# Performance work log

Measured on AMD Instinct MI355X. Metric: run time of the kernel, lower is better.

The kernel has to match this reference:

```python
import jax, jax.numpy as jnp
import numpy as np

B, S, E, H = 2, 2048, 1024, 16
D = E // H  # head_dim = 64

def setup_inputs() -> dict:
    key = jax.random.key(0)
    ks = jax.random.split(key, 11)
    s = 1.0 / np.sqrt(E)
    inp = {
        'query': jax.random.normal(ks[0], (B, S, E), jnp.float32),
        'key':   jax.random.normal(ks[1], (B, S, E), jnp.float32),
        'value': jax.random.normal(ks[2], (B, S, E), jnp.float32),
        'Wq': jax.random.uniform(ks[3], (E, E), jnp.float32, -s, s),
        'bq': jax.random.uniform(ks[4], (E,), jnp.float32, -s, s),
        'Wk': jax.random.uniform(ks[5], (E, E), jnp.float32, -s, s),
        'bk': jax.random.uniform(ks[6], (E,), jnp.float32, -s, s),
        'Wv': jax.random.uniform(ks[7], (E, E), jnp.float32, -s, s),
        'bv': jax.random.uniform(ks[8], (E,), jnp.float32, -s, s),
        'Wo': jax.random.uniform(ks[9], (E, E), jnp.float32, -s, s),
        'bo': jax.random.uniform(ks[10], (E,), jnp.float32, -s, s),
    }
    return inp

def reference(query, key, value, Wq, bq, Wk, bk, Wv, bv, Wo, bo):
    # project and split heads: [B,S,E] -> [B,H,S,D]
    def proj(x, W, b):
        y = jnp.einsum('bse,fe->bsf', x, W) + b  # torch Linear: x @ W.T + b
        return y.reshape(B, S, H, D).transpose(0, 2, 1, 3)
    q = proj(query, Wq, bq)
    k = proj(key, Wk, bk)
    v = proj(value, Wv, bv)
    scores = jnp.einsum('bhqd,bhkd->bhqk', q, k) / jnp.sqrt(jnp.float32(D))
    attn = jax.nn.softmax(scores, axis=-1)
    out = jnp.einsum('bhqk,bhkd->bhqd', attn, v)  # [B,H,S,D]
    out = out.transpose(0, 2, 1, 3).reshape(B, S, E)
    return jnp.einsum('bse,fe->bsf', out, Wo) + bo
```

## Files before the change

### kernel.cpp

```cpp
#include <hip/hip_runtime.h>

#define B_ 2
#define S_ 2048
#define E_ 1024
#define H_ 16
#define D_ 64
#define M_ (B_*S_)
#define K_ E_

typedef __attribute__((ext_vector_type(8))) short  short8;
typedef __attribute__((ext_vector_type(4))) float  f32x4;
typedef __attribute__((ext_vector_type(8))) unsigned short u16x8;
typedef __attribute__((ext_vector_type(4))) unsigned short u16x4;
typedef __attribute__((ext_vector_type(4))) unsigned int   u32x4;

#define QSCALE 0.18033688011112042f

#if __has_builtin(__builtin_amdgcn_exp2f)
#define EXP2F(x) __builtin_amdgcn_exp2f(x)
#else
#define EXP2F(x) exp2f(x)
#endif

__device__ __forceinline__ unsigned short f2bf(float f) {
    unsigned u = __float_as_uint(f);
    u += 0x7fffu + ((u >> 16) & 1u);
    return (unsigned short)(u >> 16);
}

__device__ __forceinline__ unsigned cvtpk(float a, float b) {
    unsigned r;
    asm("v_cvt_pk_bf16_f32 %0, %1, %2" : "=v"(r) : "v"(a), "v"(b));
    return r;
}

__device__ __forceinline__ void gl_lds16(const ushort* g, ushort* l) {
    __builtin_amdgcn_global_load_lds((const __attribute__((address_space(1))) void*)g,
                                     (__attribute__((address_space(3))) void*)l,
                                     16, 0, 0);
}

#define FL_SYNC(N) do {                                                   \
    asm volatile("s_waitcnt vmcnt(" #N ")" ::: "memory");                 \
    __builtin_amdgcn_s_barrier();                                         \
    asm volatile("" ::: "memory");                                        \
} while (0)

#define WAITL0_BAR() do {                                                 \
    asm volatile("s_waitcnt lgkmcnt(0)" ::: "memory");                    \
    __builtin_amdgcn_s_barrier();                                         \
    asm volatile("" ::: "memory");                                        \
} while (0)

__global__ __launch_bounds__(256)
void cvt_all(const float* __restrict__ q, const float* __restrict__ k,
             const float* __restrict__ v, const float* __restrict__ wq,
             const float* __restrict__ wk, const float* __restrict__ wv,
             const float* __restrict__ wo, ushort* __restrict__ dst)
{
    const int bid = blockIdx.x;
    const float* src;
    size_t dof;
    int local;
    if (bid < 6144) {
        const int t = bid >> 11;
        src = (t == 0) ? q : (t == 1) ? k : v;
        dof = (size_t)t * 4194304u;
        local = bid & 2047;
    } else {
        const int r = bid - 6144;
        const int t = r >> 9;
        src = (t == 0) ? wq : (t == 1) ? wk : (t == 2) ? wv : wo;
        dof = 12582912u + (size_t)t * 1048576u;
        local = r & 511;
    }
    const size_t idx = (size_t)local * 2048 + threadIdx.x * 8;
    const float4 a = *(const float4*)(src + idx);
    const float4 b = *(const float4*)(src + idx + 4);
    u16x8 o;
    o[0] = f2bf(a.x); o[1] = f2bf(a.y); o[2] = f2bf(a.z); o[3] = f2bf(a.w);
    o[4] = f2bf(b.x); o[5] = f2bf(b.y); o[6] = f2bf(b.z); o[7] = f2bf(b.w);
    *(u16x8*)(dst + dof + idx) = o;
}

template<int SWAP>
__device__ __forceinline__ void qkv_core(const ushort* __restrict__ X,
                                         const ushort* __restrict__ W,
                                         int m0, int n0,
                                         f32x4 acc[8][4], ushort* sh)
{
    const int tid  = threadIdx.x;
    const int lane = tid & 63;
    const int w    = tid >> 6;
    const int wm   = w & 1;
    const int wn   = w >> 1;
    const int l15  = lane & 15, quad = lane >> 4;

    const int srow = lane >> 3, schunk = lane & 7;
    const int scol = (schunk ^ srow) * 8;
    const ushort* pa[4]; const ushort* pb[4]; int loff[4];
    #pragma unroll
    for (int i = 0; i < 4; ++i) {
        const int row = (w * 4 + i) * 8 + srow;
        pa[i] = X + (size_t)(m0 + row) * K_ + scol;
        pb[i] = W + (size_t)(n0 + row) * K_ + scol;
        loff[i] = (w * 4 + i) * 512 + lane * 8;
    }

    const f32x4 zero = {0.f, 0.f, 0.f, 0.f};
    #pragma unroll
    for (int mt = 0; mt < 8; ++mt)
        #pragma unroll
        for (int nt = 0; nt < 4; ++nt) acc[mt][nt] = zero;

    #pragma unroll
    for (int i = 0; i < 4; ++i) {
        gl_lds16(pa[i],      sh + loff[i]);
        gl_lds16(pb[i],      sh + 16384 + loff[i]);
    }
    #pragma unroll
    for (int i = 0; i < 4; ++i) {
        gl_lds16(pa[i] + 64, sh + 32768 + loff[i]);
        gl_lds16(pb[i] + 64, sh + 32768 + 16384 + loff[i]);
    }

    const int arow = wm * 128 + l15;
    const int brow = wn * 64 + l15;

    for (int t = 0; t < 16; ++t) {
        ushort* curA = sh + (t & 1) * 32768;
        ushort* curB = curA + 16384;

        if (t < 15) { FL_SYNC(8); } else { FL_SYNC(0); }

        __builtin_amdgcn_s_setprio(1);
        #pragma unroll
        for (int kc = 0; kc < 2; ++kc) {
            short8 bf[4];
            #pragma unroll
            for (int nt = 0; nt < 4; ++nt) {
                const int r = brow + nt * 16;
                bf[nt] = *(const short8*)(curB + r * 64 + (((kc * 4 + quad) ^ (r & 7)) * 8));
            }
            #pragma unroll
            for (int mt = 0; mt < 8; ++mt) {
                const int r = arow + mt * 16;
                const short8 af = *(const short8*)(curA + r * 64 + (((kc * 4 + quad) ^ (r & 7)) * 8));
                #pragma unroll
                for (int nt = 0; nt < 4; ++nt) {
                    if (SWAP)
                        acc[mt][nt] = __builtin_amdgcn_mfma_f32_16x16x32_bf16(bf[nt], af, acc[mt][nt], 0, 0, 0);
                    else
                        acc[mt][nt] = __builtin_amdgcn_mfma_f32_16x16x32_bf16(af, bf[nt], acc[mt][nt], 0, 0, 0);
                }
            }
        }
        __builtin_amdgcn_s_setprio(0);

        if (t + 2 < 16) {
            WAITL0_BAR();
            const int k0 = (t + 2) * 64;
            #pragma unroll
            for (int i = 0; i < 4; ++i) {
                gl_lds16(pa[i] + k0, curA + loff[i]);
                gl_lds16(pb[i] + k0, curB + loff[i]);
            }
        }
    }
}

__global__ __launch_bounds__(512, 2)
void gemm_qkv(const ushort* __restrict__ Xq, const ushort* __restrict__ Xk,
              const ushort* __restrict__ Xv, const ushort* __restrict__ Wq,
              const ushort* __restrict__ Wk, const ushort* __restrict__ Wv,
              const float* __restrict__ bq, const float* __restrict__ bk,
              const float* __restrict__ bv, ushort* __restrict__ Qh,
              ushort* __restrict__ Kh, ushort* __restrict__ Vt)
{
    __shared__ ushort sh[65536];
    const int z = blockIdx.z;
    const ushort* X = (z == 0) ? Xq : (z == 1) ? Xk : Xv;
    const ushort* W = (z == 0) ? Wq : (z == 1) ? Wk : Wv;
    const float* bias = (z == 0) ? bq : (z == 1) ? bk : bv;
    ushort* dst = (z == 0) ? Qh : (z == 1) ? Kh : Vt;

    const int m0 = blockIdx.y * 256, n0 = blockIdx.x * 256;
    f32x4 acc[8][4];
    const int lane = threadIdx.x & 63, w = threadIdx.x >> 6;
    const int wm = w & 1, wn = w >> 1;
    const int l15 = lane & 15, quad = lane >> 4;

    if (z < 2) {
        qkv_core<1>(X, W, m0, n0, acc, sh);
        const float qsc = (z == 0) ? QSCALE : 1.0f;
        #pragma unroll
        for (int nt = 0; nt < 4; ++nt) {
            const int nb = n0 + wn * 64 + nt * 16 + quad * 4;
            const int h = nb >> 6, d0 = nb & 63;
            const float4 b4 = *(const float4*)(bias + nb);
            const float bb4[4] = {b4.x, b4.y, b4.z, b4.w};
            #pragma unroll
            for (int mt = 0; mt < 8; ++mt) {
                const int tok = m0 + wm * 128 + mt * 16 + l15;
                const int b = tok >> 11, s = tok & (S_ - 1);
                u16x4 pk;
                #pragma unroll
                for (int r = 0; r < 4; ++r)
                    pk[r] = f2bf((acc[mt][nt][r] + bb4[r]) * qsc);
                *(u16x4*)&dst[(((size_t)(b * H_ + h) * S_) + s) * D_ + d0] = pk;
            }
        }
    } else {
        qkv_core<0>(X, W, m0, n0, acc, sh);
        float bias4[4];
        #pragma unroll
        for (int nt = 0; nt < 4; ++nt)
            bias4[nt] = bias[n0 + wn * 64 + nt * 16 + l15];
        #pragma unroll
        for (int mt = 0; mt < 8; ++mt) {
            const int mrow0 = m0 + wm * 128 + mt * 16 + (quad * 4);
            const int b = mrow0 >> 11;
            const int s0 = mrow0 & (S_ - 1);
            #pragma unroll
            for (int nt = 0; nt < 4; ++nt) {
                const int n = n0 + wn * 64 + nt * 16 + l15;
                const int h = n >> 6, d = n & 63;
                u16x4 pk;
                #pragma unroll
                for (int r = 0; r < 4; ++r) pk[r] = f2bf(acc[mt][nt][r] + bias4[nt]);
                *(u16x4*)&Vt[(((size_t)(b * H_ + h) * D_) + d) * S_ + s0] = pk;
            }
        }
    }
}

__global__ __launch_bounds__(256)
void gemm_out(const ushort* __restrict__ X, const ushort* __restrict__ W,
              const float* __restrict__ bias, float* __restrict__ out)
{
    __shared__ ushort sh[24576];
    const int m0 = blockIdx.y * 128, n0 = blockIdx.x * 64;
    const int tid = threadIdx.x, lane = tid & 63, w = tid >> 6;
    const int wm = w & 1, wn = w >> 1;
    const int l15 = lane & 15, quad = lane >> 4;
    const int r0 = tid >> 2, c8 = (tid & 3) * 8;
    const int kb = quad * 8;

    const ushort* ga = X + (size_t)(m0 + r0) * K_ + c8;
    const ushort* gb = W + (size_t)(n0 + r0) * K_ + c8;

    const f32x4 zero = {0.f, 0.f, 0.f, 0.f};
    f32x4 acc[4][2];
    #pragma unroll
    for (int mt = 0; mt < 4; ++mt)
        #pragma unroll
        for (int nt = 0; nt < 2; ++nt) acc[mt][nt] = zero;

    #pragma unroll
    for (int t0 = 0; t0 < 2; ++t0) {
        ushort* sb = sh + t0 * 6144;
        gl_lds16(ga + t0 * 32,                 sb + tid * 8);
        gl_lds16(ga + t0 * 32 + (size_t)64 * K_, sb + 2048 + tid * 8);
        gl_lds16(gb + t0 * 32,                 sb + 4096 + tid * 8);
    }

    for (int t = 0; t < 32; ++t) {
        ushort* sb = sh + (t & 3) * 6144;

        if (t < 31) { FL_SYNC(3); } else { FL_SYNC(0); }

        short8 af[4], bf[2];
        #pragma unroll
        for (int mt = 0; mt < 4; ++mt)
            af[mt] = *(const short8*)(sb + (wm * 64 + mt * 16 + l15) * 32 + kb);
        #pragma unroll
        for (int nt = 0; nt < 2; ++nt)
            bf[nt] = *(const short8*)(sb + 4096 + (wn * 32 + nt * 16 + l15) * 32 + kb);

        if (t + 2 < 32) {
            ushort* nb = sh + ((t + 2) & 3) * 6144;
            const int k0 = (t + 2) * 32;
            gl_lds16(ga + k0,                 nb + tid * 8);
            gl_lds16(ga + k0 + (size_t)64 * K_, nb + 2048 + tid * 8);
            gl_lds16(gb + k0,                 nb + 4096 + tid * 8);
        }

        __builtin_amdgcn_s_setprio(1);
        #pragma unroll
        for (int mt = 0; mt < 4; ++mt)
            #pragma unroll
            for (int nt = 0; nt < 2; ++nt)
                acc[mt][nt] = __builtin_amdgcn_mfma_f32_16x16x32_bf16(af[mt], bf[nt], acc[mt][nt], 0, 0, 0);
        __builtin_amdgcn_s_setprio(0);
    }

    float bias2[2];
    #pragma unroll
    for (int nt = 0; nt < 2; ++nt)
        bias2[nt] = bias[n0 + wn * 32 + nt * 16 + l15];

    #pragma unroll
    for (int mt = 0; mt < 4; ++mt) {
        const int mrow0 = m0 + wm * 64 + mt * 16 + quad * 4;
        #pragma unroll
        for (int nt = 0; nt < 2; ++nt) {
            const int n = n0 + wn * 32 + nt * 16 + l15;
            #pragma unroll
            for (int r = 0; r < 4; ++r)
                out[(size_t)(mrow0 + r) * E_ + n] = acc[mt][nt][r] + bias2[nt];
        }
    }
}

#define NTILE (S_ / 64)
#define QBLK 128

__device__ __forceinline__ void flash_stage(const ushort* __restrict__ Kg,
                                            const ushort* __restrict__ Vg,
                                            size_t qk_off, size_t vt_off,
                                            ushort* sh, int j,
                                            int row0, int gcol0, int row1, int gcol1,
                                            int chunk0, int chunk1, int lane)
{
    ushort* sb = sh + 8192 + (j & 3) * 8192;
    const int j0n = j * 64;
    gl_lds16(Kg + qk_off + (size_t)(j0n + row0) * D_ + gcol0 * 8, sb + chunk0 * 512 + lane * 8);
    gl_lds16(Vg + vt_off + (size_t)row0 * S_ + j0n + gcol0 * 8, sb + 4096 + chunk0 * 512 + lane * 8);
    gl_lds16(Kg + qk_off + (size_t)(j0n + row1) * D_ + gcol1 * 8, sb + chunk1 * 512 + lane * 8);
    gl_lds16(Vg + vt_off + (size_t)row1 * S_ + j0n + gcol1 * 8, sb + 4096 + chunk1 * 512 + lane * 8);
}

__global__ __launch_bounds__(256, 2)
void flash_mfma(const ushort* __restrict__ Qg, const ushort* __restrict__ Kg,
                const ushort* __restrict__ Vg, ushort* __restrict__ AO)
{
    __shared__ ushort sh[40960];
    ushort* Qs = sh;

    const int tid = threadIdx.x, lane = tid & 63, w = tid >> 6;
    const int l15 = lane & 15, quad = lane >> 4;
    const int q0 = blockIdx.x * QBLK, h = blockIdx.y, b = blockIdx.z;
    const size_t qk_off = (size_t)(b * H_ + h) * S_ * D_;
    const size_t vt_off = (size_t)(b * H_ + h) * D_ * S_;

    const int chunk0 = w, chunk1 = w + 4;
    const int row0 = chunk0 * 8 + (lane >> 3);
    const int row1 = chunk1 * 8 + (lane >> 3);
    const int gcol0 = (lane & 7) ^ (row0 & 7);
    const int gcol1 = (lane & 7) ^ (row1 & 7);

    #pragma unroll
    for (int i = 0; i < 4; ++i) {
        const int qc = w + i * 4;
        const int qrow = qc * 8 + (lane >> 3);
        const int qg = (lane & 7) ^ (qrow & 7);
        gl_lds16(Qg + qk_off + (size_t)(q0 + qrow) * D_ + qg * 8,
                 Qs + qc * 512 + lane * 8);
    }
    flash_stage(Kg, Vg, qk_off, vt_off, sh, 0, row0, gcol0, row1, gcol1, chunk0, chunk1, lane);
    flash_stage(Kg, Vg, qk_off, vt_off, sh, 1, row0, gcol0, row1, gcol1, chunk0, chunk1, lane);

    FL_SYNC(8);

    f32x4 o[4][4];
    #pragma unroll
    for (int g = 0; g < 4; ++g)
        #pragma unroll
        for (int nt = 0; nt < 4; ++nt) o[g][nt] = {0.f, 0.f, 0.f, 0.f};
    float lsum[4] = {0.f, 0.f, 0.f, 0.f};

    const int qh  = (w >> 1) * 64;
    const int kvb = (w & 1) * 32;
    const int x7  = l15 & 7;
    const int rowA = (kvb + l15) * 64;
    const int rowB = (kvb + 16 + l15) * 64;
    const int gA = ((w & 1) * 4 + (quad >> 1)) ^ x7;
    const int gB = ((w & 1) * 4 + 2 + (quad >> 1)) ^ x7;
    const f32x4 zero = {0.f, 0.f, 0.f, 0.f};

    for (int j = 0; j < NTILE; ++j) {
        const ushort* Kb = sh + 8192 + (j & 3) * 8192;
        const ushort* Vb = Kb + 4096;
        if (j < NTILE - 1) { FL_SYNC(4); } else { FL_SYNC(0); }

        const short8 ka0 = *(const short8*)&Kb[rowA + ((quad ^ x7) * 8)];
        const short8 ka1 = *(const short8*)&Kb[rowA + (((4 + quad) ^ x7) * 8)];
        const short8 ka2 = *(const short8*)&Kb[rowB + ((quad ^ x7) * 8)];
        const short8 ka3 = *(const short8*)&Kb[rowB + (((4 + quad) ^ x7) * 8)];
        uint2 vvA[4], vvB[4];
        #pragma unroll
        for (int nt = 0; nt < 4; ++nt) {
            vvA[nt] = *(const uint2*)&Vb[(nt * 16 + l15) * 64 + gA * 8 + (quad & 1) * 4];
            vvB[nt] = *(const uint2*)&Vb[(nt * 16 + l15) * 64 + gB * 8 + (quad & 1) * 4];
        }

        if (j < NTILE - 2)
            flash_stage(Kg, Vg, qk_off, vt_off, sh, j + 2,
                        row0, gcol0, row1, gcol1, chunk0, chunk1, lane);

        __builtin_amdgcn_s_setprio(1);
        uint2 paLo[4], paHi[4];
        #pragma unroll
        for (int g = 0; g < 4; ++g) {
            const int qr = (qh + g * 16 + l15) * 64;
            const short8 qg0 = *(const short8*)&Qs[qr + ((quad ^ x7) * 8)];
            const short8 qg1 = *(const short8*)&Qs[qr + (((4 + quad) ^ x7) * 8)];
            f32x4 t = __builtin_amdgcn_mfma_f32_16x16x32_bf16(ka0, qg0, zero, 0, 0, 0);
            t = __builtin_amdgcn_mfma_f32_16x16x32_bf16(ka1, qg1, t, 0, 0, 0);
            f32x4 u = __builtin_amdgcn_mfma_f32_16x16x32_bf16(ka2, qg0, zero, 0, 0, 0);
            u = __builtin_amdgcn_mfma_f32_16x16x32_bf16(ka3, qg1, u, 0, 0, 0);
            {
                const float p0 = EXP2F(t[0]), p1 = EXP2F(t[1]);
                const float p2 = EXP2F(t[2]), p3 = EXP2F(t[3]);
                lsum[g] += (p0 + p1) + (p2 + p3);
                paLo[g].x = cvtpk(p0, p1);
                paLo[g].y = cvtpk(p2, p3);
            }
            {
                const float p0 = EXP2F(u[0]), p1 = EXP2F(u[1]);
                const float p2 = EXP2F(u[2]), p3 = EXP2F(u[3]);
                lsum[g] += (p0 + p1) + (p2 + p3);
                paHi[g].x = cvtpk(p0, p1);
                paHi[g].y = cvtpk(p2, p3);
            }
        }

        short8 pa8[4];
        #pragma unroll
        for (int g = 0; g < 4; ++g) {
            u32x4 pk;
            pk[0] = paLo[g].x; pk[1] = paLo[g].y;
            pk[2] = paHi[g].x; pk[3] = paHi[g].y;
            pa8[g] = __builtin_bit_cast(short8, pk);
        }
        #pragma unroll
        for (int nt = 0; nt < 4; ++nt) {
            u32x4 vk;
            vk[0] = vvA[nt].x; vk[1] = vvA[nt].y;
            vk[2] = vvB[nt].x; vk[3] = vvB[nt].y;
            const short8 vb8 = __builtin_bit_cast(short8, vk);
            #pragma unroll
            for (int g = 0; g < 4; ++g)
                o[g][nt] = __builtin_amdgcn_mfma_f32_16x16x32_bf16(pa8[g], vb8, o[g][nt], 0, 0, 0);
        }
        __builtin_amdgcn_s_setprio(0);
    }

    #pragma unroll
    for (int g = 0; g < 4; ++g) {
        lsum[g] += __shfl_xor(lsum[g], 16);
        lsum[g] += __shfl_xor(lsum[g], 32);
    }
    __syncthreads();
    float* fb = (float*)sh;
    if (w & 1) {
        #pragma unroll
        for (int g = 0; g < 4; ++g) {
            #pragma unroll
            for (int nt = 0; nt < 4; ++nt)
                #pragma unroll
                for (int r = 0; r < 4; ++r)
                    fb[(w >> 1) * 4096 + g * 1024 + (nt * 4 + r) * 64 + lane] = o[g][nt][r];
            if (quad == 0) fb[8192 + (w >> 1) * 64 + g * 16 + l15] = lsum[g];
        }
    }
    __syncthreads();
    if (!(w & 1)) {
        #pragma unroll
        for (int g = 0; g < 4; ++g) {
            #pragma unroll
            for (int nt = 0; nt < 4; ++nt)
                #pragma unroll
                for (int r = 0; r < 4; ++r)
                    o[g][nt][r] += fb[(w >> 1) * 4096 + g * 1024 + (nt * 4 + r) * 64 + lane];
            lsum[g] += fb[8192 + (w >> 1) * 64 + g * 16 + l15];
        }
        #pragma unroll
        for (int g = 0; g < 4; ++g) {
            const float inv = 1.0f / lsum[g];
            float invr[4];
            #pragma unroll
            for (int r = 0; r < 4; ++r)
                invr[r] = __shfl(inv, (lane & 0x30) | (quad * 4 + r));
            #pragma unroll
            for (int nt = 0; nt < 4; ++nt) {
                const int e = h * 64 + nt * 16 + l15;
                #pragma unroll
                for (int r = 0; r < 4; ++r) {
                    const int s = q0 + qh + g * 16 + quad * 4 + r;
                    AO[(size_t)(b * S_ + s) * E_ + e] = f2bf(o[g][nt][r] * invr[r]);
                }
            }
        }
    }
}

extern "C" void kernel_launch(void* const* d_in, const int* in_sizes, int n_in,
                              void* d_out, int out_size, void* d_ws, size_t ws_size,
                              hipStream_t stream) {
    const float* query = (const float*)d_in[0];
    const float* key   = (const float*)d_in[1];
    const float* value = (const float*)d_in[2];
    const float* Wq = (const float*)d_in[3];
    const float* bq = (const float*)d_in[4];
    const float* Wk = (const float*)d_in[5];
    const float* bk = (const float*)d_in[6];
    const float* Wv = (const float*)d_in[7];
    const float* bv = (const float*)d_in[8];
    const float* Wo = (const float*)d_in[9];
    const float* bo = (const float*)d_in[10];
    float* out = (float*)d_out;

    ushort* ws = (ushort*)d_ws;
    ushort* Xq  = ws;
    ushort* Xk  = ws + 4194304u;
    ushort* Xv  = ws + 8388608u;
    ushort* Wqb = ws + 12582912u;
    ushort* Wkb = ws + 13631488u;
    ushort* Wvb = ws + 14680064u;
    ushort* Wob = ws + 15728640u;
    ushort* Qh  = ws + 16777216u;
    ushort* Kh  = ws + 20971520u;
    ushort* Vt  = ws + 25165824u;
    ushort* AO  = ws + 29360128u;

    cvt_all<<<8192, 256, 0, stream>>>(query, key, value, Wq, Wk, Wv, Wo, ws);
    gemm_qkv<<<dim3(4, 16, 3), 512, 0, stream>>>(Xq, Xk, Xv, Wqb, Wkb, Wvb,
                                                 bq, bk, bv, Qh, Kh, Vt);
    flash_mfma<<<dim3(S_ / QBLK, H_, B_), 256, 0, stream>>>(Qh, Kh, Vt, AO);
    gemm_out<<<dim3(16, 32), 256, 0, stream>>>(AO, Wob, bo, out);
}
```

Baseline: 210.0 us.

## Switch QKV GEMM to 4-stage K=32 LDS ring with early prefetch

The QKV projection GEMM mainloop moves from a double-buffered K=64 tile to a four-slot ring of K=32 tiles. Each iteration now loads all A/B fragments into registers first, then issues the global-to-LDS prefetch for stage t+2, then runs the MFMAs. This removes the trailing wait-and-barrier before each prefetch and lets loads overlap compute more. In exchange there are twice as many iterations and more sync points, and the fragments held in registers raise register pressure.

```diff
diff --git a/kernel.cpp b/kernel.cpp
--- a/kernel.cpp
+++ b/kernel.cpp
@@ -83,6 +83,15 @@
     *(u16x8*)(dst + dof + idx) = o;
 }
 
+#define QKV_STAGE(t) do {                                                  \
+    ushort* sb_ = sh + ((t) & 3) * 16384;                                  \
+    const int k0_ = (t) * 32;                                              \
+    gl_lds16(pa0 + k0_, sb_ + ld0);                                        \
+    gl_lds16(pa1 + k0_, sb_ + 4096 + ld0);                                 \
+    gl_lds16(pb0 + k0_, sb_ + 8192 + ld0);                                 \
+    gl_lds16(pb1 + k0_, sb_ + 12288 + ld0);                                \
+} while (0)
+
 template<int SWAP>
 __device__ __forceinline__ void qkv_core(const ushort* __restrict__ X,
                                          const ushort* __restrict__ W,
@@ -96,16 +105,13 @@
     const int wn   = w >> 1;
     const int l15  = lane & 15, quad = lane >> 4;
 
-    const int srow = lane >> 3, schunk = lane & 7;
-    const int scol = (schunk ^ srow) * 8;
-    const ushort* pa[4]; const ushort* pb[4]; int loff[4];
-    #pragma unroll
-    for (int i = 0; i < 4; ++i) {
-        const int row = (w * 4 + i) * 8 + srow;
-        pa[i] = X + (size_t)(m0 + row) * K_ + scol;
-        pb[i] = W + (size_t)(n0 + row) * K_ + scol;
-        loff[i] = (w * 4 + i) * 512 + lane * 8;
-    }
+    const int srow = tid >> 2, cidx = tid & 3;
+    const int scol = (cidx ^ (srow & 3)) * 8;
+    const ushort* pa0 = X + (size_t)(m0 + srow) * K_ + scol;
+    const ushort* pa1 = X + (size_t)(m0 + 128 + srow) * K_ + scol;
+    const ushort* pb0 = W + (size_t)(n0 + srow) * K_ + scol;
+    const ushort* pb1 = W + (size_t)(n0 + 128 + srow) * K_ + scol;
+    const int ld0 = tid * 8;
 
     const f32x4 zero = {0.f, 0.f, 0.f, 0.f};
     #pragma unroll
@@ -113,59 +119,40 @@
         #pragma unroll
         for (int nt = 0; nt < 4; ++nt) acc[mt][nt] = zero;
 
-    #pragma unroll
-    for (int i = 0; i < 4; ++i) {
-        gl_lds16(pa[i],      sh + loff[i]);
-        gl_lds16(pb[i],      sh + 16384 + loff[i]);
-    }
-    #pragma unroll
-    for (int i = 0; i < 4; ++i) {
-        gl_lds16(pa[i] + 64, sh + 32768 + loff[i]);
-        gl_lds16(pb[i] + 64, sh + 32768 + 16384 + loff[i]);
-    }
-
+    QKV_STAGE(0);
+    QKV_STAGE(1);
+
+    const int xq = (quad ^ (l15 & 3)) * 8;
     const int arow = wm * 128 + l15;
     const int brow = wn * 64 + l15;
 
-    for (int t = 0; t < 16; ++t) {
-        ushort* curA = sh + (t & 1) * 32768;
-        ushort* curB = curA + 16384;
-
-        if (t < 15) { FL_SYNC(8); } else { FL_SYNC(0); }
+    for (int t = 0; t < 32; ++t) {
+        ushort* sb = sh + (t & 3) * 16384;
+
+        if (t < 31) { FL_SYNC(4); } else { FL_SYNC(0); }
+
+        short8 bf[4];
+        #pragma unroll
+        for (int nt = 0; nt < 4; ++nt)
+            bf[nt] = *(const short8*)(sb + 8192 + (brow + nt * 16) * 32 + xq);
+        short8 af[8];
+        #pragma unroll
+        for (int mt = 0; mt < 8; ++mt)
+            af[mt] = *(const short8*)(sb + (arow + mt * 16) * 32 + xq);
+
+        if (t + 2 < 32) QKV_STAGE(t + 2);
 
         __builtin_amdgcn_s_setprio(1);
         #pragma unroll
-        for (int kc = 0; kc < 2; ++kc) {
-            short8 bf[4];
+        for (int mt = 0; mt < 8; ++mt)
             #pragma unroll
             for (int nt = 0; nt < 4; ++nt) {
-                const int r = brow + nt * 16;
-                bf[nt] = *(const short8*)(curB + r * 64 + (((kc * 4 + quad) ^ (r & 7)) * 8));
+                if (SWAP)
+                    acc[mt][nt] = __builtin_amdgcn_mfma_f32_16x16x32_bf16(bf[nt], af[mt], acc[mt][nt], 0, 0, 0);
+                else
+                    acc[mt][nt] = __builtin_amdgcn_mfma_f32_16x16x32_bf16(af[mt], bf[nt], acc[mt][nt], 0, 0, 0);
             }
-            #pragma unroll
-            for (int mt = 0; mt < 8; ++mt) {
-                const int r = arow + mt * 16;
-                const short8 af = *(const short8*)(curA + r * 64 + (((kc * 4 + quad) ^ (r & 7)) * 8));
-                #pragma unroll
-                for (int nt = 0; nt < 4; ++nt) {
-                    if (SWAP)
-                        acc[mt][nt] = __builtin_amdgcn_mfma_f32_16x16x32_bf16(bf[nt], af, acc[mt][nt], 0, 0, 0);
-                    else
-                        acc[mt][nt] = __builtin_amdgcn_mfma_f32_16x16x32_bf16(af, bf[nt], acc[mt][nt], 0, 0, 0);
-                }
-            }
-        }
         __builtin_amdgcn_s_setprio(0);
-
-        if (t + 2 < 16) {
-            WAITL0_BAR();
-            const int k0 = (t + 2) * 64;
-            #pragma unroll
-            for (int i = 0; i < 4; ++i) {
-                gl_lds16(pa[i] + k0, curA + loff[i]);
-                gl_lds16(pb[i] + k0, curB + loff[i]);
-            }
-        }
     }
 }
 
```

Result: no change. 208.0 us (-0.9%).
